# Performance work log

Hardware: AMD Instinct MI355X
Metric: run time of the kernel (lower is better)

Reference implementation:

```python
import jax, jax.numpy as jnp
import numpy as np

N = 8192        # nodes in batch
E = 262144      # edges (avg degree 32)
IN_C = 64
OUT_C = 64
K = 3           # max_k
G = 64          # graphs in batch
NC = 10         # n_class
EPS = 1e-5      # batchnorm eps


def setup_inputs() -> dict:
    key = jax.random.key(0)
    ks = jax.random.split(key, 16)
    D_in = IN_C * K    # 192
    D_out = OUT_C * K  # 192
    inp = {
        'x': jax.random.normal(ks[0], (N, IN_C), jnp.float32),
        'edge_index': jax.random.randint(ks[1], (2, E), 0, N, dtype=jnp.int64),
        'batch': jnp.sort(jax.random.randint(ks[2], (N,), 0, G, dtype=jnp.int64)),
        # spectral-normed masked linear
        'W_orig': jax.random.normal(ks[3], (D_out, D_in), jnp.float32) * 0.05,
        'b': jnp.zeros((D_out,), jnp.float32),
        'u': jax.random.normal(ks[4], (D_out,), jnp.float32),
        # batchnorms (training-mode batch stats)
        'bn1_gamma': jnp.ones((D_out,), jnp.float32),
        'bn1_beta': jnp.zeros((D_out,), jnp.float32),
        'bn2_gamma': jnp.ones((D_out * 3,), jnp.float32),
        'bn2_beta': jnp.zeros((D_out * 3,), jnp.float32),
        # funnel head
        'w1': jax.random.normal(ks[5], (D_out * 2, D_out * 3), jnp.float32) * 0.05,
        'b1': jnp.zeros((D_out * 2,), jnp.float32),
        'w2': jax.random.normal(ks[6], (D_out, D_out * 2), jnp.float32) * 0.05,
        'b2': jnp.zeros((D_out,), jnp.float32),
        'w3': jax.random.normal(ks[7], (NC, D_out), jnp.float32) * 0.05,
        'b3': jnp.zeros((NC,), jnp.float32),
    }
    return inp


def _forward(x, edge_index, batch, W_orig, b, u, bn1_gamma, bn1_beta,
             bn2_gamma, bn2_beta, w1, b1, w2, b2, w3, b3):
    n = x.shape[0]
    row, col = edge_index[0], edge_index[1]
    # sym-normalized Laplacian L = I - D^-1/2 A D^-1/2, densified ([N,N])
    deg = jnp.zeros((n,), x.dtype).at[row].add(1.0)
    dinv = jnp.where(deg > 0, jax.lax.rsqrt(jnp.maximum(deg, 1.0)), 0.0)
    vals = -dinv[row] * dinv[col]
    L = jnp.zeros((n, n), x.dtype).at[row, col].add(vals)
    idx = jnp.arange(n)
    L = L.at[idx, idx].add(1.0)
    Hs = [x]
    h = x
    for _ in range(K - 1):
        h = L @ h
        Hs.append(h)
    Hcat = jnp.concatenate(Hs, axis=1)              # [N, IN_C*K]
    # spectral norm of W (one power-iteration step with stored u)
    v = W_orig.T @ u
    v = v / (jnp.linalg.norm(v) + 1e-12)
    sigma = u @ (W_orig @ v)
    W = W_orig / sigma
    # block lower-triangular mask: block i passes first IN_C*(i+1) input cols
    col_idx = jnp.arange(IN_C * K)
    row_block = jnp.arange(OUT_C * K) // OUT_C
    mask = (col_idx[None, :] < IN_C * (row_block[:, None] + 1)).astype(W.dtype)
    H = Hcat @ (W * mask).T + b                     # masked linear
    # reservoir_act_fun is identity (default)
    mu, var = H.mean(0), H.var(0)                   # BN (batch stats)
    H = bn1_gamma * (H - mu) * jax.lax.rsqrt(var + EPS) + bn1_beta
    # fused-style triple pooling over graph ids
    Hsum = jax.ops.segment_sum(H, batch, num_segments=G)
    cnt = jax.ops.segment_sum(jnp.ones((n,), H.dtype), batch, num_segments=G)
    Havg = Hsum / jnp.maximum(cnt, 1.0)[:, None]
    Hmax = jax.ops.segment_max(H, batch, num_segments=G)
    Hg = jnp.concatenate([Havg, Hsum, Hmax], axis=1)  # [G, 3*OUT_C*K]
    mu2, var2 = Hg.mean(0), Hg.var(0)
    xo = bn2_gamma * (Hg - mu2) * jax.lax.rsqrt(var2 + EPS) + bn2_beta
    # funnel output (dropout = identity in eval)
    xo = jax.nn.relu(xo @ w1.T + b1)
    xo = jax.nn.relu(xo @ w2.T + b2)
    return jax.nn.log_softmax(xo @ w3.T + b3, axis=1)


def reference(x, edge_index, batch, W_orig, b, u, bn1_gamma, bn1_beta,
              bn2_gamma, bn2_beta, w1, b1, w2, b2, w3, b3):
    return _forward(x, edge_index, batch, W_orig, b, u, bn1_gamma, bn1_beta,
                    bn2_gamma, bn2_beta, w1, b1, w2, b2, w3, b3)
```

## Files before the change

### kernel.cpp

```cpp
#include <hip/hip_runtime.h>
#include <math.h>

#define NN   8192
#define EE   262144
#define CIN  64
#define DD   192
#define GG   64
#define NCLS 10
#define D3   576
#define F1   384
#define F2   192
#define EPSB 1e-5f
#define NB   64
#define EPB  (EE / NB)

__device__ __forceinline__ unsigned int fkey(float f) {
    unsigned int b = __float_as_uint(f);
    return b ^ (0x80000000u | (unsigned int)((int)b >> 31));
}
__device__ __forceinline__ float fdec(unsigned int k) {
    unsigned int b = k ^ ((k & 0x80000000u) ? 0x80000000u : 0xFFFFFFFFu);
    return __uint_as_float(b);
}

__global__ __launch_bounds__(1024) void prep_kernel(const float* __restrict__ W,
    const float* __restrict__ u, const float* __restrict__ w1,
    const float* __restrict__ w2, const int* __restrict__ batch,
    const int* __restrict__ ei,
    float* __restrict__ sig, int* __restrict__ gstart,
    unsigned short* __restrict__ pcnt,
    float* __restrict__ Wp, float* __restrict__ Wp1, float* __restrict__ Wp2,
    int* __restrict__ pinit) {
    __shared__ int hist[NN];
    int b = blockIdx.x, t = threadIdx.x;
    if (b < 324) {
        int idx = b * 1024 + t;
        if (idx < DD * DD) {
            int r = idx / DD, c = idx - r * DD;
            float m = (c < CIN * ((r >> 6) + 1)) ? 1.f : 0.f;
            Wp[((c >> 2) * DD + r) * 4 + (c & 3)] = m * W[idx];
        } else if (idx < DD * DD + F1 * D3) {
            int i1 = idx - DD * DD;
            int tt = i1 / D3, k = i1 - tt * D3;
            Wp1[((k >> 2) * F1 + tt) * 4 + (k & 3)] = w1[i1];
        } else {
            int i2 = idx - DD * DD - F1 * D3;
            int tt = i2 / F1, k = i2 - tt * F1;
            Wp2[((k >> 2) * F2 + tt) * 4 + (k & 3)] = w2[i2];
        }
        return;
    }
    if (b == 325) {
        for (int i = t; i < NN; i += 1024) {
            int b0 = batch[i];
            int b1 = (i + 1 < NN) ? batch[i + 1] : GG;
            if (i == 0) { for (int g = 0; g <= b0; g++) gstart[g] = 0; }
            for (int g = b0 + 1; g <= b1; g++) gstart[g] = i + 1;
        }
        return;
    }
    if (b == 326 + NB) {
        int4* z = (int4*)pinit;
        for (int i = t; i < 3 * GG * DD / 4; i += 1024) z[i] = make_int4(0, 0, 0, 0);
        int4* m = (int4*)(pinit + 3 * GG * DD);
        for (int i = t; i < GG * DD / 4; i += 1024) m[i] = make_int4(-1, -1, -1, -1);
        return;
    }
    if (b >= 326) {
        int cb = b - 326;
        int4* hz = (int4*)hist;
        for (int i = t; i < NN / 4; i += 1024) hz[i] = make_int4(0, 0, 0, 0);
        __syncthreads();
        int e0 = cb * EPB;
        for (int i = t; i < EPB; i += 1024) atomicAdd(&hist[ei[e0 + i]], 1);
        __syncthreads();
        const int2* h2 = (const int2*)hist;
        ushort2* q2 = (ushort2*)&pcnt[cb * NN];
        for (int i = t; i < NN / 2; i += 1024) {
            int2 h = h2[i];
            q2[i] = make_ushort2((unsigned short)h.x, (unsigned short)h.y);
        }
        return;
    }
    float* vp  = (float*)hist;
    float* vsh = vp + 768;
    float* red = vsh + DD;
    if (t < 768) {
        int c = t >> 2, j = t & 3;
        float s = 0.f;
        const float* Wc = W + c;
        for (int i = j * 48; i < j * 48 + 48; i++) s += Wc[i * DD] * u[i];
        vp[t] = s;
    }
    __syncthreads();
    float vv = 0.f;
    if (t < DD) {
        float v = vp[4 * t] + vp[4 * t + 1] + vp[4 * t + 2] + vp[4 * t + 3];
        vsh[t] = v;
        vv = v * v;
    }
    red[t] = vv;
    __syncthreads();
    for (int off = 512; off > 0; off >>= 1) {
        if (t < off) red[t] += red[t + off];
        __syncthreads();
    }
    float norm = sqrtf(red[0]) + 1e-12f;
    __syncthreads();
    float a = 0.f;
    for (int idx = t; idx < DD * DD; idx += 1024) {
        int r = idx / DD, c = idx - r * DD;
        a += u[r] * W[idx] * vsh[c];
    }
    red[t] = a;
    __syncthreads();
    for (int off = 512; off > 0; off >>= 1) {
        if (t < off) red[t] += red[t + off];
        __syncthreads();
    }
    if (t == 0) sig[0] = norm / red[0];
}

__global__ __launch_bounds__(256) void offs_kernel(unsigned short* __restrict__ pcnt,
                                                   int* __restrict__ deg,
                                                   float* __restrict__ dinv) {
    int i = blockIdx.x * 256 + threadIdx.x;
    int run = 0;
#pragma unroll
    for (int b = 0; b < NB; b++) {
        int v = pcnt[b * NN + i];
        pcnt[b * NN + i] = (unsigned short)run;
        run += v;
    }
    deg[i] = run;
    dinv[i] = (run > 0) ? rsqrtf((float)run) : 0.f;
}

__global__ __launch_bounds__(1024) void scatter_kernel(const int* __restrict__ ei,
                                                       const int* __restrict__ deg,
                                                       const unsigned short* __restrict__ off,
                                                       int* __restrict__ rowptr,
                                                       unsigned short* __restrict__ csr_col) {
    __shared__ int cur[NN];
    __shared__ int temp[1024];
    int b = blockIdx.x, t = threadIdx.x;
    int base = t * 8;
    int d[8], l[8];
    {
        const int4 a4 = *(const int4*)&deg[base];
        const int4 b4 = *(const int4*)&deg[base + 4];
        d[0] = a4.x; d[1] = a4.y; d[2] = a4.z; d[3] = a4.w;
        d[4] = b4.x; d[5] = b4.y; d[6] = b4.z; d[7] = b4.w;
    }
    int run = 0;
#pragma unroll
    for (int j = 0; j < 8; j++) { l[j] = run; run += d[j]; }
    temp[t] = run;
    __syncthreads();
    for (int o = 1; o < 1024; o <<= 1) {
        int v = (t >= o) ? temp[t - o] : 0;
        __syncthreads();
        temp[t] += v;
        __syncthreads();
    }
    int prefix = (t > 0) ? temp[t - 1] : 0;
    {
        const unsigned short* ob = &off[b * NN];
        int4 opk = *(const int4*)(ob + base);
        cur[base + 0] = prefix + l[0] + (opk.x & 0xFFFF);
        cur[base + 1] = prefix + l[1] + (int)((unsigned)opk.x >> 16);
        cur[base + 2] = prefix + l[2] + (opk.y & 0xFFFF);
        cur[base + 3] = prefix + l[3] + (int)((unsigned)opk.y >> 16);
        cur[base + 4] = prefix + l[4] + (opk.z & 0xFFFF);
        cur[base + 5] = prefix + l[5] + (int)((unsigned)opk.z >> 16);
        cur[base + 6] = prefix + l[6] + (opk.w & 0xFFFF);
        cur[base + 7] = prefix + l[7] + (int)((unsigned)opk.w >> 16);
    }
    if (b == 0) {
#pragma unroll
        for (int j = 0; j < 8; j++) rowptr[base + j] = prefix + l[j];
        if (t == 1023) rowptr[NN] = temp[1023];
    }
    __syncthreads();
    int e0 = b * EPB;
    for (int i = t; i < EPB; i += 1024) {
        int r = ei[e0 + i];
        int c = ei[EE + e0 + i];
        int pos = atomicAdd(&cur[r], 1);
        csr_col[pos] = (unsigned short)c;
    }
}

__global__ __launch_bounds__(256) void spmm_kernel(const float* __restrict__ in,
    const int* __restrict__ rowptr, const unsigned short* __restrict__ col,
    const float* __restrict__ dinv, float* __restrict__ outb) {
    int idx = blockIdx.x * 256 + threadIdx.x;
    int row = idx >> 6;
    int lane = idx & 63;
    int s = rowptr[row], e = rowptr[row + 1];
    float acc0 = 0.f, acc1 = 0.f, acc2 = 0.f, acc3 = 0.f;
    int p = s;
    for (; p + 3 < e; p += 4) {
        int c0 = col[p], c1 = col[p + 1], c2 = col[p + 2], c3 = col[p + 3];
        acc0 += dinv[c0] * in[c0 * 64 + lane];
        acc1 += dinv[c1] * in[c1 * 64 + lane];
        acc2 += dinv[c2] * in[c2 * 64 + lane];
        acc3 += dinv[c3] * in[c3 * 64 + lane];
    }
    for (; p < e; p++) {
        int c = col[p];
        acc0 += dinv[c] * in[c * 64 + lane];
    }
    float acc = (acc0 + acc1) + (acc2 + acc3);
    float self = in[row * 64 + lane];
    outb[row * 64 + lane] = self - dinv[row] * acc;
}

__global__ __launch_bounds__(384) void gemm_pool_kernel(const float* __restrict__ x,
    const float* __restrict__ Hx1, const float* __restrict__ Hx2,
    const float* __restrict__ Wp, const float* __restrict__ bias,
    const float* __restrict__ sig, const int* __restrict__ batch,
    float* __restrict__ Psum, float* __restrict__ Psq,
    unsigned int* __restrict__ Pmaxk, unsigned int* __restrict__ Pmink) {
    __shared__ float hs[16 * DD];
    __shared__ int bb[16];
    int t = threadIdx.x;
    int n0 = blockIdx.x * 16;
    for (int i = t; i < 768; i += 384) {
        int r = i / 48, q = i - r * 48;
        float4 v;
        if (q < 16)      v = ((const float4*)x)[(n0 + r) * 16 + q];
        else if (q < 32) v = ((const float4*)Hx1)[(n0 + r) * 16 + (q - 16)];
        else             v = ((const float4*)Hx2)[(n0 + r) * 16 + (q - 32)];
        *(float4*)&hs[r * DD + q * 4] = v;
    }
    if (t < 16) bb[t] = batch[n0 + t];
    __syncthreads();
    int half = t / 192;
    int ch = t - half * 192;
    int r0 = half * 8;
    float acc[8];
#pragma unroll
    for (int r = 0; r < 8; r++) acc[r] = 0.f;
    const float4* Wp4 = (const float4*)Wp;
    const float* hb = &hs[r0 * DD];
    for (int k4 = 0; k4 < DD / 4; k4++) {
        float4 w = Wp4[k4 * DD + ch];
#pragma unroll
        for (int r = 0; r < 8; r++) {
            const float4 h = *(const float4*)&hb[r * DD + k4 * 4];
            acc[r] += h.x * w.x + h.y * w.y + h.z * w.z + h.w * w.w;
        }
    }
    float inv_sigma = sig[0];
    float bv = bias[ch];
    int gcur = bb[r0];
    float sum = 0.f, sq = 0.f, mn = INFINITY, mx = -INFINITY;
#pragma unroll
    for (int r = 0; r < 8; r++) {
        float v = inv_sigma * acc[r] + bv;
        int g = bb[r0 + r];
        if (g != gcur) {
            atomicAdd(&Psum[gcur * DD + ch], sum);
            atomicAdd(&Psq[gcur * DD + ch], sq);
            atomicMax(&Pmaxk[gcur * DD + ch], fkey(mx));
            atomicMin(&Pmink[gcur * DD + ch], fkey(mn));
            sum = 0.f; sq = 0.f; mn = INFINITY; mx = -INFINITY; gcur = g;
        }
        sum += v; sq += v * v;
        mn = fminf(mn, v); mx = fmaxf(mx, v);
    }
    atomicAdd(&Psum[gcur * DD + ch], sum);
    atomicAdd(&Psq[gcur * DD + ch], sq);
    atomicMax(&Pmaxk[gcur * DD + ch], fkey(mx));
    atomicMin(&Pmink[gcur * DD + ch], fkey(mn));
}

__global__ __launch_bounds__(64) void hg_kernel(
    const float* __restrict__ Psum, const float* __restrict__ Psq,
    const unsigned int* __restrict__ Pmaxk, const unsigned int* __restrict__ Pmink,
    const int* __restrict__ gstart,
    const float* __restrict__ g1, const float* __restrict__ be1,
    const float* __restrict__ g2, const float* __restrict__ be2,
    float* __restrict__ Hg) {
    int t = blockIdx.x;
    int g = threadIdx.x;
    int f = t / DD, c = t - f * DD;
    float Sg = Psum[g * DD + c];
    float Qg = Psq[g * DD + c];
    float S = Sg, Q = Qg;
    for (int off = 32; off > 0; off >>= 1) {
        S += __shfl_xor(S, off);
        Q += __shfl_xor(Q, off);
    }
    float mu = S * (1.f / (float)NN);
    float var = Q * (1.f / (float)NN) - mu * mu;
    float sc = g1[c] * rsqrtf(var + EPSB);
    float bb = be1[c];
    float v;
    if (f == 2) {
        float mx = fdec(Pmaxk[g * DD + c]);
        float mn = fdec(Pmink[g * DD + c]);
        float raw = (sc >= 0.f) ? mx : mn;
        v = sc * (raw - mu) + bb;
    } else {
        float nf = (float)(gstart[g + 1] - gstart[g]);
        float hsum = sc * (Sg - nf * mu) + nf * bb;
        v = (f == 0) ? hsum / fmaxf(nf, 1.f) : hsum;
    }
    float s2 = v, ss2 = v * v;
    for (int off = 32; off > 0; off >>= 1) {
        s2 += __shfl_xor(s2, off);
        ss2 += __shfl_xor(ss2, off);
    }
    float m2 = s2 * (1.f / (float)GG);
    float var2 = ss2 * (1.f / (float)GG) - m2 * m2;
    float sc2 = g2[t] * rsqrtf(var2 + EPSB);
    Hg[g * D3 + t] = sc2 * (v - m2) + be2[t];
}

__global__ __launch_bounds__(F1) void funnel_kernel(const float* __restrict__ Hg,
    const float* __restrict__ Wp1, const float* __restrict__ b1,
    const float* __restrict__ Wp2, const float* __restrict__ b2,
    const float* __restrict__ w3, const float* __restrict__ b3,
    float* __restrict__ out) {
    __shared__ float hg[D3];
    __shared__ float x1[F1];
    __shared__ float x2[F2];
    __shared__ float lg[NCLS];
    __shared__ float s_lse;
    int g = blockIdx.x, t = threadIdx.x;
    for (int i = t; i < D3; i += F1) hg[i] = Hg[g * D3 + i];
    __syncthreads();
    {
        float a = b1[t];
        const float4* W4 = (const float4*)Wp1;
        for (int k4 = 0; k4 < D3 / 4; k4++) {
            float4 w = W4[k4 * F1 + t];
            const float4 h = *(const float4*)&hg[k4 * 4];
            a += w.x * h.x + w.y * h.y + w.z * h.z + w.w * h.w;
        }
        x1[t] = fmaxf(a, 0.f);
    }
    __syncthreads();
    if (t < F2) {
        float a = b2[t];
        const float4* W4 = (const float4*)Wp2;
        for (int k4 = 0; k4 < F1 / 4; k4++) {
            float4 w = W4[k4 * F2 + t];
            const float4 h = *(const float4*)&x1[k4 * 4];
            a += w.x * h.x + w.y * h.y + w.z * h.z + w.w * h.w;
        }
        x2[t] = fmaxf(a, 0.f);
    }
    __syncthreads();
    if (t < NCLS) {
        float a = b3[t];
        const float4* wr = (const float4*)&w3[t * F2];
        const float4* h4 = (const float4*)x2;
        for (int k = 0; k < F2 / 4; k++) {
            float4 w = wr[k], h = h4[k];
            a += w.x * h.x + w.y * h.y + w.z * h.z + w.w * h.w;
        }
        lg[t] = a;
    }
    __syncthreads();
    if (t == 0) {
        float m = lg[0];
        for (int i = 1; i < NCLS; i++) m = fmaxf(m, lg[i]);
        float se = 0.f;
        for (int i = 0; i < NCLS; i++) se += expf(lg[i] - m);
        s_lse = m + logf(se);
    }
    __syncthreads();
    if (t < NCLS) out[g * NCLS + t] = lg[t] - s_lse;
}


extern "C" void kernel_launch(void* const* d_in, const int* in_sizes, int n_in,
                              void* d_out, int out_size, void* d_ws, size_t ws_size,
                              hipStream_t stream) {
    (void)in_sizes; (void)n_in; (void)out_size; (void)ws_size;
    const float* x     = (const float*)d_in[0];
    const int*   ei    = (const int*)d_in[1];
    const int*   batch = (const int*)d_in[2];
    const float* W     = (const float*)d_in[3];
    const float* b     = (const float*)d_in[4];
    const float* u     = (const float*)d_in[5];
    const float* g1    = (const float*)d_in[6];
    const float* be1   = (const float*)d_in[7];
    const float* g2    = (const float*)d_in[8];
    const float* be2   = (const float*)d_in[9];
    const float* w1    = (const float*)d_in[10];
    const float* b1    = (const float*)d_in[11];
    const float* w2    = (const float*)d_in[12];
    const float* b2    = (const float*)d_in[13];
    const float* w3    = (const float*)d_in[14];
    const float* b3    = (const float*)d_in[15];
    float* out = (float*)d_out;
    char*  ws  = (char*)d_ws;

    int*            gstart  = (int*)(ws + 0);
    int*            rowptr  = (int*)(ws + 512);
    int*            deg     = (int*)(ws + 33536);
    float*          dinv    = (float*)(ws + 66304);
    float*          sig     = (float*)(ws + 99072);
    float*          Wp      = (float*)(ws + 99328);
    float*          Psum    = (float*)(ws + 246784);
    float*          Psq     = (float*)(ws + 295936);
    unsigned int*   Pmaxk   = (unsigned int*)(ws + 345088);
    unsigned int*   Pmink   = (unsigned int*)(ws + 394240);
    float*          Hg      = (float*)(ws + 443392);
    unsigned short* csr_col = (unsigned short*)(ws + 590848);
    float*          Wp1     = (float*)(ws + 1115136);
    float*          Wp2     = (float*)(ws + 1999872);
    unsigned short* pcnt    = (unsigned short*)(ws + 2294784);
    float*          Hx1     = (float*)(ws + 3343360);
    float*          Hx2     = (float*)(ws + 5440512);

    prep_kernel<<<326 + NB + 1, 1024, 0, stream>>>(W, u, w1, w2, batch, ei,
                                                   sig, gstart, pcnt, Wp, Wp1, Wp2,
                                                   (int*)Psum);
    offs_kernel<<<NN / 256, 256, 0, stream>>>(pcnt, deg, dinv);
    scatter_kernel<<<NB, 1024, 0, stream>>>(ei, deg, pcnt, rowptr, csr_col);
    spmm_kernel<<<NN * 64 / 256, 256, 0, stream>>>(x, rowptr, csr_col, dinv, Hx1);
    spmm_kernel<<<NN * 64 / 256, 256, 0, stream>>>(Hx1, rowptr, csr_col, dinv, Hx2);
    gemm_pool_kernel<<<NN / 16, 384, 0, stream>>>(x, Hx1, Hx2, Wp, b, sig, batch,
                                                  Psum, Psq, Pmaxk, Pmink);
    hg_kernel<<<D3, 64, 0, stream>>>(Psum, Psq, Pmaxk, Pmink, gstart, g1, be1, g2, be2, Hg);
    funnel_kernel<<<GG, F1, 0, stream>>>(Hg, Wp1, b1, Wp2, b2, w3, b3, out);
}
```

Before: 179.8 us.

## Fuse degree offsets into scatter and BN/pooling finalize into funnel kernel

Removes the offs_kernel by having each scatter block read all per-block counts, computing the degree and its own exclusive offset, with block 0 writing dinv. Removes hg_kernel by having each funnel block recompute the batchnorm statistics and pooled features for its graph from Psum/Psq/Pmax/Pmin. Two launches and the deg/Hg intermediates go away, but the work becomes redundant: every scatter block reads the full count array, and every funnel block repeats the 64-graph reductions serially per channel, which lengthens the funnel's critical path.

```diff
diff --git a/kernel.cpp b/kernel.cpp
--- a/kernel.cpp
+++ b/kernel.cpp
@@ -121,64 +121,48 @@
     if (t == 0) sig[0] = norm / red[0];
 }
 
-__global__ __launch_bounds__(256) void offs_kernel(unsigned short* __restrict__ pcnt,
-                                                   int* __restrict__ deg,
-                                                   float* __restrict__ dinv) {
-    int i = blockIdx.x * 256 + threadIdx.x;
-    int run = 0;
-#pragma unroll
-    for (int b = 0; b < NB; b++) {
-        int v = pcnt[b * NN + i];
-        pcnt[b * NN + i] = (unsigned short)run;
-        run += v;
-    }
-    deg[i] = run;
-    dinv[i] = (run > 0) ? rsqrtf((float)run) : 0.f;
-}
-
 __global__ __launch_bounds__(1024) void scatter_kernel(const int* __restrict__ ei,
-                                                       const int* __restrict__ deg,
-                                                       const unsigned short* __restrict__ off,
+                                                       const unsigned short* __restrict__ pcnt,
                                                        int* __restrict__ rowptr,
+                                                       float* __restrict__ dinv,
                                                        unsigned short* __restrict__ csr_col) {
     __shared__ int cur[NN];
     __shared__ int temp[1024];
     int b = blockIdx.x, t = threadIdx.x;
     int base = t * 8;
-    int d[8], l[8];
-    {
-        const int4 a4 = *(const int4*)&deg[base];
-        const int4 b4 = *(const int4*)&deg[base + 4];
-        d[0] = a4.x; d[1] = a4.y; d[2] = a4.z; d[3] = a4.w;
-        d[4] = b4.x; d[5] = b4.y; d[6] = b4.z; d[7] = b4.w;
-    }
-    int run = 0;
-#pragma unroll
-    for (int j = 0; j < 8; j++) { l[j] = run; run += d[j]; }
+    int dg[8] = {0, 0, 0, 0, 0, 0, 0, 0};
+    int o[8] = {0, 0, 0, 0, 0, 0, 0, 0};
+    for (int bp = 0; bp < NB; bp++) {
+        int4 pk = *(const int4*)&pcnt[bp * NN + base];
+        if (bp == b) {
+#pragma unroll
+            for (int j = 0; j < 8; j++) o[j] = dg[j];
+        }
+        dg[0] += (pk.x & 0xFFFF); dg[1] += (int)((unsigned)pk.x >> 16);
+        dg[2] += (pk.y & 0xFFFF); dg[3] += (int)((unsigned)pk.y >> 16);
+        dg[4] += (pk.z & 0xFFFF); dg[5] += (int)((unsigned)pk.z >> 16);
+        dg[6] += (pk.w & 0xFFFF); dg[7] += (int)((unsigned)pk.w >> 16);
+    }
+    int run = 0, l[8];
+#pragma unroll
+    for (int j = 0; j < 8; j++) { l[j] = run; run += dg[j]; }
     temp[t] = run;
     __syncthreads();
-    for (int o = 1; o < 1024; o <<= 1) {
-        int v = (t >= o) ? temp[t - o] : 0;
+    for (int oo = 1; oo < 1024; oo <<= 1) {
+        int v = (t >= oo) ? temp[t - oo] : 0;
         __syncthreads();
         temp[t] += v;
         __syncthreads();
     }
     int prefix = (t > 0) ? temp[t - 1] : 0;
-    {
-        const unsigned short* ob = &off[b * NN];
-        int4 opk = *(const int4*)(ob + base);
-        cur[base + 0] = prefix + l[0] + (opk.x & 0xFFFF);
-        cur[base + 1] = prefix + l[1] + (int)((unsigned)opk.x >> 16);
-        cur[base + 2] = prefix + l[2] + (opk.y & 0xFFFF);
-        cur[base + 3] = prefix + l[3] + (int)((unsigned)opk.y >> 16);
-        cur[base + 4] = prefix + l[4] + (opk.z & 0xFFFF);
-        cur[base + 5] = prefix + l[5] + (int)((unsigned)opk.z >> 16);
-        cur[base + 6] = prefix + l[6] + (opk.w & 0xFFFF);
-        cur[base + 7] = prefix + l[7] + (int)((unsigned)opk.w >> 16);
-    }
+#pragma unroll
+    for (int j = 0; j < 8; j++) cur[base + j] = prefix + l[j] + o[j];
     if (b == 0) {
 #pragma unroll
-        for (int j = 0; j < 8; j++) rowptr[base + j] = prefix + l[j];
+        for (int j = 0; j < 8; j++) {
+            rowptr[base + j] = prefix + l[j];
+            dinv[base + j] = (dg[j] > 0) ? rsqrtf((float)dg[j]) : 0.f;
+        }
         if (t == 1023) rowptr[NN] = temp[1023];
     }
     __syncthreads();
@@ -276,50 +260,12 @@
     atomicMin(&Pmink[gcur * DD + ch], fkey(mn));
 }
 
-__global__ __launch_bounds__(64) void hg_kernel(
+__global__ __launch_bounds__(F1) void funnel_kernel(
     const float* __restrict__ Psum, const float* __restrict__ Psq,
     const unsigned int* __restrict__ Pmaxk, const unsigned int* __restrict__ Pmink,
     const int* __restrict__ gstart,
     const float* __restrict__ g1, const float* __restrict__ be1,
     const float* __restrict__ g2, const float* __restrict__ be2,
-    float* __restrict__ Hg) {
-    int t = blockIdx.x;
-    int g = threadIdx.x;
-    int f = t / DD, c = t - f * DD;
-    float Sg = Psum[g * DD + c];
-    float Qg = Psq[g * DD + c];
-    float S = Sg, Q = Qg;
-    for (int off = 32; off > 0; off >>= 1) {
-        S += __shfl_xor(S, off);
-        Q += __shfl_xor(Q, off);
-    }
-    float mu = S * (1.f / (float)NN);
-    float var = Q * (1.f / (float)NN) - mu * mu;
-    float sc = g1[c] * rsqrtf(var + EPSB);
-    float bb = be1[c];
-    float v;
-    if (f == 2) {
-        float mx = fdec(Pmaxk[g * DD + c]);
-        float mn = fdec(Pmink[g * DD + c]);
-        float raw = (sc >= 0.f) ? mx : mn;
-        v = sc * (raw - mu) + bb;
-    } else {
-        float nf = (float)(gstart[g + 1] - gstart[g]);
-        float hsum = sc * (Sg - nf * mu) + nf * bb;
-        v = (f == 0) ? hsum / fmaxf(nf, 1.f) : hsum;
-    }
-    float s2 = v, ss2 = v * v;
-    for (int off = 32; off > 0; off >>= 1) {
-        s2 += __shfl_xor(s2, off);
-        ss2 += __shfl_xor(ss2, off);
-    }
-    float m2 = s2 * (1.f / (float)GG);
-    float var2 = ss2 * (1.f / (float)GG) - m2 * m2;
-    float sc2 = g2[t] * rsqrtf(var2 + EPSB);
-    Hg[g * D3 + t] = sc2 * (v - m2) + be2[t];
-}
-
-__global__ __launch_bounds__(F1) void funnel_kernel(const float* __restrict__ Hg,
     const float* __restrict__ Wp1, const float* __restrict__ b1,
     const float* __restrict__ Wp2, const float* __restrict__ b2,
     const float* __restrict__ w3, const float* __restrict__ b3,
@@ -329,8 +275,42 @@
     __shared__ float x2[F2];
     __shared__ float lg[NCLS];
     __shared__ float s_lse;
+    __shared__ float nfs[GG];
     int g = blockIdx.x, t = threadIdx.x;
-    for (int i = t; i < D3; i += F1) hg[i] = Hg[g * D3 + i];
+    if (t < GG) nfs[t] = (float)(gstart[t + 1] - gstart[t]);
+    __syncthreads();
+    for (int c = t; c < D3; c += F1) {
+        int f = c / DD, cc = c - f * DD;
+        float S = 0.f, Q = 0.f;
+        for (int gp = 0; gp < GG; gp++) {
+            S += Psum[gp * DD + cc];
+            Q += Psq[gp * DD + cc];
+        }
+        float mu = S * (1.f / (float)NN);
+        float var = Q * (1.f / (float)NN) - mu * mu;
+        float sc = g1[cc] * rsqrtf(var + EPSB);
+        float bb = be1[cc];
+        float s2 = 0.f, ss2 = 0.f, vown = 0.f;
+        for (int gp = 0; gp < GG; gp++) {
+            float v;
+            if (f == 2) {
+                float mx = fdec(Pmaxk[gp * DD + cc]);
+                float mn = fdec(Pmink[gp * DD + cc]);
+                float raw = (sc >= 0.f) ? mx : mn;
+                v = sc * (raw - mu) + bb;
+            } else {
+                float nf = nfs[gp];
+                float hsum = sc * (Psum[gp * DD + cc] - nf * mu) + nf * bb;
+                v = (f == 0) ? hsum / fmaxf(nf, 1.f) : hsum;
+            }
+            s2 += v; ss2 += v * v;
+            if (gp == g) vown = v;
+        }
+        float m2 = s2 * (1.f / (float)GG);
+        float var2 = ss2 * (1.f / (float)GG) - m2 * m2;
+        float sc2 = g2[c] * rsqrtf(var2 + EPSB);
+        hg[c] = sc2 * (vown - m2) + be2[c];
+    }
     __syncthreads();
     {
         float a = b1[t];
@@ -402,31 +382,29 @@
 
     int*            gstart  = (int*)(ws + 0);
     int*            rowptr  = (int*)(ws + 512);
-    int*            deg     = (int*)(ws + 33536);
-    float*          dinv    = (float*)(ws + 66304);
-    float*          sig     = (float*)(ws + 99072);
-    float*          Wp      = (float*)(ws + 99328);
-    float*          Psum    = (float*)(ws + 246784);
-    float*          Psq     = (float*)(ws + 295936);
-    unsigned int*   Pmaxk   = (unsigned int*)(ws + 345088);
-    unsigned int*   Pmink   = (unsigned int*)(ws + 394240);
-    float*          Hg      = (float*)(ws + 443392);
-    unsigned short* csr_col = (unsigned short*)(ws + 590848);
-    float*          Wp1     = (float*)(ws + 1115136);
-    float*          Wp2     = (float*)(ws + 1999872);
-    unsigned short* pcnt    = (unsigned short*)(ws + 2294784);
-    float*          Hx1     = (float*)(ws + 3343360);
-    float*          Hx2     = (float*)(ws + 5440512);
+    float*          dinv    = (float*)(ws + 33536);
+    float*          sig     = (float*)(ws + 66304);
+    float*          Wp      = (float*)(ws + 66560);
+    float*          Psum    = (float*)(ws + 214016);
+    float*          Psq     = (float*)(ws + 263168);
+    unsigned int*   Pmaxk   = (unsigned int*)(ws + 312320);
+    unsigned int*   Pmink   = (unsigned int*)(ws + 361472);
+    unsigned short* csr_col = (unsigned short*)(ws + 410624);
+    float*          Wp1     = (float*)(ws + 934912);
+    float*          Wp2     = (float*)(ws + 1819648);
+    unsigned short* pcnt    = (unsigned short*)(ws + 2114560);
+    float*          Hx1     = (float*)(ws + 3163136);
+    float*          Hx2     = (float*)(ws + 5260288);
 
     prep_kernel<<<326 + NB + 1, 1024, 0, stream>>>(W, u, w1, w2, batch, ei,
                                                    sig, gstart, pcnt, Wp, Wp1, Wp2,
                                                    (int*)Psum);
-    offs_kernel<<<NN / 256, 256, 0, stream>>>(pcnt, deg, dinv);
-    scatter_kernel<<<NB, 1024, 0, stream>>>(ei, deg, pcnt, rowptr, csr_col);
+    scatter_kernel<<<NB, 1024, 0, stream>>>(ei, pcnt, rowptr, dinv, csr_col);
     spmm_kernel<<<NN * 64 / 256, 256, 0, stream>>>(x, rowptr, csr_col, dinv, Hx1);
     spmm_kernel<<<NN * 64 / 256, 256, 0, stream>>>(Hx1, rowptr, csr_col, dinv, Hx2);
     gemm_pool_kernel<<<NN / 16, 384, 0, stream>>>(x, Hx1, Hx2, Wp, b, sig, batch,
                                                   Psum, Psq, Pmaxk, Pmink);
-    hg_kernel<<<D3, 64, 0, stream>>>(Psum, Psq, Pmaxk, Pmink, gstart, g1, be1, g2, be2, Hg);
-    funnel_kernel<<<GG, F1, 0, stream>>>(Hg, Wp1, b1, Wp2, b2, w3, b3, out);
-}
+    funnel_kernel<<<GG, F1, 0, stream>>>(Psum, Psq, Pmaxk, Pmink, gstart,
+                                         g1, be1, g2, be2,
+                                         Wp1, b1, Wp2, b2, w3, b3, out);
+}
```

New measurement: 216.9 us. 1.21x slower.
